# Performance work log

Measured on AMD Instinct MI355X. Metric: run time of the kernel, lower is better.

Reference implementation:

```python
import jax, jax.numpy as jnp
import numpy as np

B, C, H, W = 8, 64, 32, 32
NEG = 256
TEMP = 2.0
FACTOR = 0.8
EPS = 1e-8


def setup_inputs() -> dict:
    key = jax.random.key(0)
    k1, k2, k3, k4 = jax.random.split(key, 4)
    views_1 = jax.random.normal(k1, (B, C, H, W), dtype=jnp.float32)
    views_2 = jax.random.normal(k2, (B, C, H, W), dtype=jnp.float32)
    img = jax.random.uniform(k3, (1, 3, H, W), dtype=jnp.float32)
    neg_idx = jax.random.randint(k4, (B, 2, H * W, NEG), 0, H, dtype=jnp.int32)
    return {"views_1": views_1, "views_2": views_2, "img": img, "neg_idx": neg_idx}


def _forward(views_1, views_2, img, neg_idx):
    hw = H * W
    height = jnp.arange(hw) // W
    width = jnp.arange(hw) % W
    coords = jnp.stack([height, width]).astype(jnp.float32)  # [2, hw]
    img0 = img[0]  # [3, H, W]; original uses img[0] for EVERY batch element
    euc_norm = jnp.sqrt(jnp.asarray((H - 1) ** 2 + (W - 1) ** 2, jnp.float32))
    sqrt3 = jnp.sqrt(jnp.asarray(3.0, jnp.float32))

    center = img0[:, height, width]  # [3, hw]

    def per_sample(z1, z2, nidx):
        # nidx: [2, hw, neg]
        nf = nidx.astype(jnp.float32)
        # torch.norm with no dim => scalar Frobenius norm over [2, neg] per pixel
        d = coords[:, :, None] - nf  # [2, hw, neg]
        euc = jnp.sqrt(jnp.sum(d * d, axis=(0, 2))) / euc_norm  # [hw]
        negs = img0[:, nidx[0], nidx[1]]  # [3, hw, neg]
        rd = center[:, :, None] - negs
        rgb = jnp.sqrt(jnp.sum(rd * rd, axis=(0, 2))) / sqrt3  # [hw]
        weight = euc * FACTOR + rgb * (1.0 - FACTOR)  # [hw], constant across neg

        z1v = z1.reshape(C, hw)  # [c, hw]
        pn = z2[:, nidx[0], nidx[1]]  # [c, hw, neg]
        dot = jnp.einsum('cp,cpn->pn', z1v, pn)  # [hw, neg]
        z1sq = jnp.sum(z1v * z1v, axis=0)  # [hw]
        z1n = jnp.sqrt(z1sq)
        pnn = jnp.sqrt(jnp.sum(pn * pn, axis=0))  # [hw, neg]
        cos = dot / jnp.maximum(z1n[:, None] * pnn, EPS)  # [hw, neg]
        cos0 = z1sq / jnp.maximum(z1sq, EPS)  # [hw] (self-similarity ~ 1)

        sim_neg = jnp.minimum(jnp.abs(cos * weight[:, None]), 1.0)  # [hw, neg]
        sim0 = jnp.minimum(jnp.abs(cos0), 1.0)  # [hw]
        sim = jnp.concatenate(
            [jnp.mean(sim0)[None], jnp.mean(sim_neg, axis=0) / TEMP]
        )  # [neg+1]

        # BCELoss with target = [1, 0, ..., 0]; torch clamps log terms at -100
        logp = jnp.maximum(jnp.log(sim[0]), -100.0)
        log1m = jnp.maximum(jnp.log1p(-sim[1:]), -100.0)
        bce = -(logp + jnp.sum(log1m)) / (NEG + 1)
        return bce, sim

    bce, sims = jax.vmap(per_sample)(views_1, views_2, neg_idx)
    loss = jnp.mean(bce)
    sim_all = jnp.sum(sims, axis=0)
    return (loss, sim_all[0] / B, jnp.sum(sim_all[1:]) / NEG * TEMP / B)


def reference(views_1, views_2, img, neg_idx):
    return _forward(views_1, views_2, img, neg_idx)
```

## Files before the change

### kernel.cpp

```cpp
#include <hip/hip_runtime.h>
#include <math.h>

#define BB 8
#define CC 64
#define HH 32
#define WW 32
#define HW 1024
#define NEGN 256
#define TEMP 2.0f
#define FACTOR 0.8f
#define EPSF 1e-8f
#define PT 8

__global__ __launch_bounds__(256) void contrastive_fused(
    const float* __restrict__ z1,
    const float* __restrict__ z2,
    const float* __restrict__ img,
    const int*   __restrict__ nidx,
    float* __restrict__ accSim,
    float* __restrict__ accSim0)
{
    __shared__ float As_s[CC * PT];
    __shared__ float Dt_s[PT * HW];
    __shared__ float normq_s[HW];
    __shared__ float imgs[3 * HW];
    __shared__ float simpart[PT * NEGN];
    __shared__ float z1sqs[PT];

    const int t  = threadIdx.x;
    const int b  = blockIdx.x >> 7;
    const int p0 = (blockIdx.x & 127) * PT;

    const int lane32 = t & 31;
    const int pp_b   = t >> 5;
    const int p_b    = p0 + pp_b;

    int rr[8], cc_[8];
    const size_t nbase = ((size_t)(b * 2) * HW + p_b) * NEGN;
    #pragma unroll
    for (int j = 0; j < 8; ++j) {
        rr[j]  = nidx[nbase + lane32 + 32 * j];
        cc_[j] = nidx[nbase + (size_t)HW * NEGN + lane32 + 32 * j];
    }

    for (int i = t; i < CC * PT; i += 256) {
        const int c = i >> 3, pp = i & 7;
        As_s[i] = z1[((size_t)(b * CC + c)) * HW + p0 + pp];
    }
    for (int i = t; i < 3 * HW; i += 256) imgs[i] = img[i];
    __syncthreads();

    if (t < PT) {
        float s = 0.f;
        #pragma unroll
        for (int c = 0; c < CC; ++c) { const float v = As_s[c * PT + t]; s += v * v; }
        z1sqs[t] = s;
    }

    const float4* __restrict__ z2f4 =
        reinterpret_cast<const float4*>(z2 + (size_t)b * CC * HW);
    float4 acc[PT];
    #pragma unroll
    for (int pp = 0; pp < PT; ++pp) acc[pp] = make_float4(0.f, 0.f, 0.f, 0.f);
    float4 sq = make_float4(0.f, 0.f, 0.f, 0.f);

    #pragma unroll 8
    for (int k = 0; k < CC; ++k) {
        const float4 bv = z2f4[k * (HW / 4) + t];
        sq.x = fmaf(bv.x, bv.x, sq.x);
        sq.y = fmaf(bv.y, bv.y, sq.y);
        sq.z = fmaf(bv.z, bv.z, sq.z);
        sq.w = fmaf(bv.w, bv.w, sq.w);
        const float4 a03 = reinterpret_cast<const float4*>(As_s)[k * 2];
        const float4 a47 = reinterpret_cast<const float4*>(As_s)[k * 2 + 1];
        const float av[8] = {a03.x, a03.y, a03.z, a03.w, a47.x, a47.y, a47.z, a47.w};
        #pragma unroll
        for (int pp = 0; pp < PT; ++pp) {
            acc[pp].x = fmaf(av[pp], bv.x, acc[pp].x);
            acc[pp].y = fmaf(av[pp], bv.y, acc[pp].y);
            acc[pp].z = fmaf(av[pp], bv.z, acc[pp].z);
            acc[pp].w = fmaf(av[pp], bv.w, acc[pp].w);
        }
    }
    float4* Dt4 = reinterpret_cast<float4*>(Dt_s);
    #pragma unroll
    for (int pp = 0; pp < PT; ++pp) Dt4[pp * (HW / 4) + t] = acc[pp];
    reinterpret_cast<float4*>(normq_s)[t] =
        make_float4(sqrtf(sq.x), sqrtf(sq.y), sqrtf(sq.z), sqrtf(sq.w));
    __syncthreads();

    const float z1sq = z1sqs[pp_b];
    const float z1n  = sqrtf(z1sq);
    const float cen0 = imgs[p_b], cen1 = imgs[HW + p_b], cen2 = imgs[2 * HW + p_b];
    const float hp = (float)(p_b >> 5), wp = (float)(p_b & 31);

    float se = 0.f, sr = 0.f;
    float cosv[8];
    #pragma unroll
    for (int j = 0; j < 8; ++j) {
        const int q = rr[j] * WW + cc_[j];
        const float dh = hp - (float)rr[j], dw = wp - (float)cc_[j];
        se += dh * dh + dw * dw;
        const float d0 = cen0 - imgs[q];
        const float d1 = cen1 - imgs[HW + q];
        const float d2 = cen2 - imgs[2 * HW + q];
        sr += d0 * d0 + d1 * d1 + d2 * d2;
        const float dot = Dt_s[pp_b * HW + q];
        const float pnn = normq_s[q];
        cosv[j] = dot / fmaxf(z1n * pnn, EPSF);
    }
    #pragma unroll
    for (int off = 16; off; off >>= 1) {
        se += __shfl_xor(se, off);
        sr += __shfl_xor(sr, off);
    }
    const float euc_norm = sqrtf((float)((HH - 1) * (HH - 1) + (WW - 1) * (WW - 1)));
    const float weight = sqrtf(se) / euc_norm * FACTOR +
                         sqrtf(sr) / sqrtf(3.0f) * (1.0f - FACTOR);
    #pragma unroll
    for (int j = 0; j < 8; ++j)
        simpart[pp_b * NEGN + lane32 + 32 * j] = fminf(fabsf(cosv[j] * weight), 1.0f);
    __syncthreads();

    float s = 0.f;
    #pragma unroll
    for (int pp = 0; pp < PT; ++pp) s += simpart[pp * NEGN + t];
    atomicAdd(accSim + b * NEGN + t, s);

    if (t < PT) {
        const float c0 = z1sq / fmaxf(z1sq, EPSF);
        float s0 = fminf(fabsf(c0), 1.0f);
        #pragma unroll
        for (int off = 4; off; off >>= 1) s0 += __shfl_xor(s0, off);
        if (t == 0) atomicAdd(accSim0 + b, s0);
    }
}

__global__ __launch_bounds__(256) void finalize(
    const float* __restrict__ accSim,
    const float* __restrict__ accSim0,
    float* __restrict__ out)
{
    const int t = threadIdx.x;
    float ssum = 0.f, lsum = 0.f;
    #pragma unroll
    for (int b = 0; b < BB; ++b) {
        const float s = accSim[b * NEGN + t] * (1.0f / HW) * (1.0f / TEMP);
        ssum += s;
        lsum += fmaxf(log1pf(-s), -100.0f);
    }
    __shared__ float rs[4], rl[4];
    #pragma unroll
    for (int off = 32; off; off >>= 1) {
        ssum += __shfl_down(ssum, off);
        lsum += __shfl_down(lsum, off);
    }
    if ((t & 63) == 0) { rs[t >> 6] = ssum; rl[t >> 6] = lsum; }
    __syncthreads();

    if (t == 0) {
        const float S = rs[0] + rs[1] + rs[2] + rs[3];
        const float L = rl[0] + rl[1] + rl[2] + rl[3];
        float logpsum = 0.f, sim0sum = 0.f;
        #pragma unroll
        for (int b = 0; b < BB; ++b) {
            const float s0 = accSim0[b] * (1.0f / HW);
            sim0sum += s0;
            logpsum += fmaxf(logf(s0), -100.0f);
        }
        out[0] = -(logpsum + L) / ((float)(NEGN + 1) * (float)BB);
        out[1] = sim0sum / (float)BB;
        out[2] = S / (float)NEGN * TEMP / (float)BB;
    }
}

extern "C" void kernel_launch(void* const* d_in, const int* in_sizes, int n_in,
                              void* d_out, int out_size, void* d_ws, size_t ws_size,
                              hipStream_t stream) {
    const float* v1   = (const float*)d_in[0];
    const float* v2   = (const float*)d_in[1];
    const float* img  = (const float*)d_in[2];
    const int*   nidx = (const int*)  d_in[3];

    float* accSim  = (float*)d_ws;
    float* accSim0 = accSim + BB * NEGN;

    hipMemsetAsync(accSim, 0, (BB * NEGN + BB) * sizeof(float), stream);

    contrastive_fused<<<BB * (HW / PT), 256, 0, stream>>>(
        v1, v2, img, nidx, accSim, accSim0);
    finalize<<<1, 256, 0, stream>>>(accSim, accSim0, (float*)d_out);
}
```

Before: 106.2 us.

## Replace atomics and memset with per-tile partials and multi-block finalize

Drops the memset and the global atomicAdds. Each tile now writes its partial similarity sums to a workspace, and a finalize kernel with one block per batch reduces them, with the last block producing the outputs through an atomic counter. The change also folds the reciprocal norms into the stored dot products, removing a per-lookup divide, and reuses shared memory between the z1 tile and the sim partials. The counter is reset inside the first kernel, which depends on kernel ordering, and the finalize reads more workspace data.

```diff
diff --git a/kernel.cpp b/kernel.cpp
--- a/kernel.cpp
+++ b/kernel.cpp
@@ -11,30 +11,38 @@
 #define FACTOR 0.8f
 #define EPSF 1e-8f
 #define PT 8
+#define NTILE 128
+
+#define WS_PART   0
+#define WS_S0PART (BB * NTILE * NEGN)
+#define WS_BRES   (WS_S0PART + BB * NTILE)
+#define WS_CNT    (WS_BRES + BB * 3)
 
 __global__ __launch_bounds__(256) void contrastive_fused(
     const float* __restrict__ z1,
     const float* __restrict__ z2,
     const float* __restrict__ img,
     const int*   __restrict__ nidx,
-    float* __restrict__ accSim,
-    float* __restrict__ accSim0)
+    float* __restrict__ ws)
 {
-    __shared__ float As_s[CC * PT];
-    __shared__ float Dt_s[PT * HW];
-    __shared__ float normq_s[HW];
-    __shared__ float imgs[3 * HW];
-    __shared__ float simpart[PT * NEGN];
-    __shared__ float z1sqs[PT];
+    __shared__ float smem[2048 + PT * HW + 3 * HW + PT];
+    float* const un    = smem;
+    float* const Dt_s  = smem + 2048;
+    float* const imgs  = Dt_s + PT * HW;
+    float* const z1sqs = imgs + 3 * HW;
 
     const int t  = threadIdx.x;
     const int b  = blockIdx.x >> 7;
-    const int p0 = (blockIdx.x & 127) * PT;
+    const int tile = blockIdx.x & (NTILE - 1);
+    const int p0 = tile * PT;
 
     const int lane32 = t & 31;
     const int pp_b   = t >> 5;
     const int p_b    = p0 + pp_b;
 
+    if (blockIdx.x == 0 && t == 0)
+        ((int*)ws)[WS_CNT] = 0;
+
     int rr[8], cc_[8];
     const size_t nbase = ((size_t)(b * 2) * HW + p_b) * NEGN;
     #pragma unroll
@@ -45,7 +53,7 @@
 
     for (int i = t; i < CC * PT; i += 256) {
         const int c = i >> 3, pp = i & 7;
-        As_s[i] = z1[((size_t)(b * CC + c)) * HW + p0 + pp];
+        un[i] = z1[((size_t)(b * CC + c)) * HW + p0 + pp];
     }
     for (int i = t; i < 3 * HW; i += 256) imgs[i] = img[i];
     __syncthreads();
@@ -53,7 +61,7 @@
     if (t < PT) {
         float s = 0.f;
         #pragma unroll
-        for (int c = 0; c < CC; ++c) { const float v = As_s[c * PT + t]; s += v * v; }
+        for (int c = 0; c < CC; ++c) { const float v = un[c * PT + t]; s += v * v; }
         z1sqs[t] = s;
     }
 
@@ -71,8 +79,8 @@
         sq.y = fmaf(bv.y, bv.y, sq.y);
         sq.z = fmaf(bv.z, bv.z, sq.z);
         sq.w = fmaf(bv.w, bv.w, sq.w);
-        const float4 a03 = reinterpret_cast<const float4*>(As_s)[k * 2];
-        const float4 a47 = reinterpret_cast<const float4*>(As_s)[k * 2 + 1];
+        const float4 a03 = reinterpret_cast<const float4*>(un)[k * 2];
+        const float4 a47 = reinterpret_cast<const float4*>(un)[k * 2 + 1];
         const float av[8] = {a03.x, a03.y, a03.z, a03.w, a47.x, a47.y, a47.z, a47.w};
         #pragma unroll
         for (int pp = 0; pp < PT; ++pp) {
@@ -82,15 +90,20 @@
             acc[pp].w = fmaf(av[pp], bv.w, acc[pp].w);
         }
     }
+    const float4 rp = make_float4(
+        1.0f / fmaxf(sqrtf(sq.x), 1e-20f), 1.0f / fmaxf(sqrtf(sq.y), 1e-20f),
+        1.0f / fmaxf(sqrtf(sq.z), 1e-20f), 1.0f / fmaxf(sqrtf(sq.w), 1e-20f));
     float4* Dt4 = reinterpret_cast<float4*>(Dt_s);
     #pragma unroll
-    for (int pp = 0; pp < PT; ++pp) Dt4[pp * (HW / 4) + t] = acc[pp];
-    reinterpret_cast<float4*>(normq_s)[t] =
-        make_float4(sqrtf(sq.x), sqrtf(sq.y), sqrtf(sq.z), sqrtf(sq.w));
+    for (int pp = 0; pp < PT; ++pp) {
+        float4 v = acc[pp];
+        v.x *= rp.x; v.y *= rp.y; v.z *= rp.z; v.w *= rp.w;
+        Dt4[pp * (HW / 4) + t] = v;
+    }
     __syncthreads();
 
     const float z1sq = z1sqs[pp_b];
-    const float z1n  = sqrtf(z1sq);
+    const float rz1  = 1.0f / fmaxf(sqrtf(z1sq), 1e-20f);
     const float cen0 = imgs[p_b], cen1 = imgs[HW + p_b], cen2 = imgs[2 * HW + p_b];
     const float hp = (float)(p_b >> 5), wp = (float)(p_b & 31);
 
@@ -105,9 +118,7 @@
         const float d1 = cen1 - imgs[HW + q];
         const float d2 = cen2 - imgs[2 * HW + q];
         sr += d0 * d0 + d1 * d1 + d2 * d2;
-        const float dot = Dt_s[pp_b * HW + q];
-        const float pnn = normq_s[q];
-        cosv[j] = dot / fmaxf(z1n * pnn, EPSF);
+        cosv[j] = Dt_s[pp_b * HW + q] * rz1;
     }
     #pragma unroll
     for (int off = 16; off; off >>= 1) {
@@ -117,60 +128,79 @@
     const float euc_norm = sqrtf((float)((HH - 1) * (HH - 1) + (WW - 1) * (WW - 1)));
     const float weight = sqrtf(se) / euc_norm * FACTOR +
                          sqrtf(sr) / sqrtf(3.0f) * (1.0f - FACTOR);
+    __syncthreads();
     #pragma unroll
     for (int j = 0; j < 8; ++j)
-        simpart[pp_b * NEGN + lane32 + 32 * j] = fminf(fabsf(cosv[j] * weight), 1.0f);
+        un[pp_b * NEGN + lane32 + 32 * j] = fminf(fabsf(cosv[j] * weight), 1.0f);
     __syncthreads();
 
     float s = 0.f;
     #pragma unroll
-    for (int pp = 0; pp < PT; ++pp) s += simpart[pp * NEGN + t];
-    atomicAdd(accSim + b * NEGN + t, s);
+    for (int pp = 0; pp < PT; ++pp) s += un[pp * NEGN + t];
+    ws[WS_PART + ((size_t)(b * NTILE + tile)) * NEGN + t] = s;
 
     if (t < PT) {
         const float c0 = z1sq / fmaxf(z1sq, EPSF);
         float s0 = fminf(fabsf(c0), 1.0f);
         #pragma unroll
         for (int off = 4; off; off >>= 1) s0 += __shfl_xor(s0, off);
-        if (t == 0) atomicAdd(accSim0 + b, s0);
+        if (t == 0) ws[WS_S0PART + b * NTILE + tile] = s0;
     }
 }
 
 __global__ __launch_bounds__(256) void finalize(
-    const float* __restrict__ accSim,
-    const float* __restrict__ accSim0,
-    float* __restrict__ out)
+    float* __restrict__ ws, float* __restrict__ out)
 {
     const int t = threadIdx.x;
-    float ssum = 0.f, lsum = 0.f;
-    #pragma unroll
-    for (int b = 0; b < BB; ++b) {
-        const float s = accSim[b * NEGN + t] * (1.0f / HW) * (1.0f / TEMP);
-        ssum += s;
-        lsum += fmaxf(log1pf(-s), -100.0f);
-    }
-    __shared__ float rs[4], rl[4];
+    const int b = blockIdx.x;
+    const float* part = ws + WS_PART + (size_t)b * NTILE * NEGN;
+
+    float s_bn = 0.f;
+    #pragma unroll 8
+    for (int tile = 0; tile < NTILE; ++tile)
+        s_bn += part[(size_t)tile * NEGN + t];
+
+    const float s = s_bn * (1.0f / HW) * (1.0f / TEMP);
+    float ssum = s;
+    float lsum = fmaxf(log1pf(-s), -100.0f);
+
+    __shared__ float rs[4], rl[4], r0[2];
     #pragma unroll
     for (int off = 32; off; off >>= 1) {
         ssum += __shfl_down(ssum, off);
         lsum += __shfl_down(lsum, off);
     }
     if ((t & 63) == 0) { rs[t >> 6] = ssum; rl[t >> 6] = lsum; }
+
+    if (t < 128) {
+        float v = ws[WS_S0PART + b * NTILE + t];
+        #pragma unroll
+        for (int off = 32; off; off >>= 1) v += __shfl_down(v, off);
+        if ((t & 63) == 0) r0[t >> 6] = v;
+    }
     __syncthreads();
 
     if (t == 0) {
-        const float S = rs[0] + rs[1] + rs[2] + rs[3];
-        const float L = rl[0] + rl[1] + rl[2] + rl[3];
-        float logpsum = 0.f, sim0sum = 0.f;
-        #pragma unroll
-        for (int b = 0; b < BB; ++b) {
-            const float s0 = accSim0[b] * (1.0f / HW);
-            sim0sum += s0;
-            logpsum += fmaxf(logf(s0), -100.0f);
+        ws[WS_BRES + b * 3 + 0] = rs[0] + rs[1] + rs[2] + rs[3];
+        ws[WS_BRES + b * 3 + 1] = rl[0] + rl[1] + rl[2] + rl[3];
+        ws[WS_BRES + b * 3 + 2] = r0[0] + r0[1];
+        __threadfence();
+        const int done = atomicAdd((int*)ws + WS_CNT, 1);
+        if (done == BB - 1) {
+            __threadfence();
+            float S = 0.f, L = 0.f, logp = 0.f, s0m = 0.f;
+            #pragma unroll
+            for (int bb = 0; bb < BB; ++bb) {
+                S += ws[WS_BRES + bb * 3 + 0];
+                L += ws[WS_BRES + bb * 3 + 1];
+                const float s0 = ws[WS_BRES + bb * 3 + 2] * (1.0f / HW);
+                s0m  += s0;
+                logp += fmaxf(logf(s0), -100.0f);
+            }
+            out[0] = -(logp + L) / ((float)(NEGN + 1) * (float)BB);
+            out[1] = s0m / (float)BB;
+            out[2] = S / (float)NEGN * TEMP / (float)BB;
         }
-        out[0] = -(logpsum + L) / ((float)(NEGN + 1) * (float)BB);
-        out[1] = sim0sum / (float)BB;
-        out[2] = S / (float)NEGN * TEMP / (float)BB;
     }
 }
 
@@ -181,13 +211,8 @@
     const float* v2   = (const float*)d_in[1];
     const float* img  = (const float*)d_in[2];
     const int*   nidx = (const int*)  d_in[3];
-
-    float* accSim  = (float*)d_ws;
-    float* accSim0 = accSim + BB * NEGN;
-
-    hipMemsetAsync(accSim, 0, (BB * NEGN + BB) * sizeof(float), stream);
-
-    contrastive_fused<<<BB * (HW / PT), 256, 0, stream>>>(
-        v1, v2, img, nidx, accSim, accSim0);
-    finalize<<<1, 256, 0, stream>>>(accSim, accSim0, (float*)d_out);
+    float* ws = (float*)d_ws;
+
+    contrastive_fused<<<BB * NTILE, 256, 0, stream>>>(v1, v2, img, nidx, ws);
+    finalize<<<BB, 256, 0, stream>>>(ws, (float*)d_out);
 }
```

New measurement: 125.1 us. 1.18x slower.

## Drop image and norm staging in LDS, prescale dots by reciprocal norms, use LDS atomics

Applied to the files above, without the earlier changes.

The image is no longer copied into shared memory; it is read directly from global memory through the cache. The per-column norm array and the division are replaced by multiplying the dot products with reciprocal norms before storing them. The per-pixel partial sims are reduced with shared-memory atomics instead of a staging buffer and an extra pass. A small init kernel also replaces the memset. Together these cut LDS footprint, which may raise occupancy, and remove copy and divide work. The cost is cached global gathers and atomic contention, and the max-with-EPS clamp semantics change slightly.

```diff
diff --git a/kernel.cpp b/kernel.cpp
--- a/kernel.cpp
+++ b/kernel.cpp
@@ -11,6 +11,13 @@
 #define FACTOR 0.8f
 #define EPSF 1e-8f
 #define PT 8
+#define NTILE 128
+
+
+__global__ __launch_bounds__(256) void init_acc(float* __restrict__ acc) {
+    const int i = blockIdx.x * 256 + threadIdx.x;
+    if (i < BB * NEGN + BB) acc[i] = 0.f;
+}
 
 __global__ __launch_bounds__(256) void contrastive_fused(
     const float* __restrict__ z1,
@@ -22,14 +29,13 @@
 {
     __shared__ float As_s[CC * PT];
     __shared__ float Dt_s[PT * HW];
-    __shared__ float normq_s[HW];
-    __shared__ float imgs[3 * HW];
-    __shared__ float simpart[PT * NEGN];
+    __shared__ float nacc[NEGN];
     __shared__ float z1sqs[PT];
 
-    const int t  = threadIdx.x;
-    const int b  = blockIdx.x >> 7;
-    const int p0 = (blockIdx.x & 127) * PT;
+    const int t    = threadIdx.x;
+    const int b    = blockIdx.x >> 7;
+    const int tile = blockIdx.x & (NTILE - 1);
+    const int p0   = tile * PT;
 
     const int lane32 = t & 31;
     const int pp_b   = t >> 5;
@@ -43,11 +49,12 @@
         cc_[j] = nidx[nbase + (size_t)HW * NEGN + lane32 + 32 * j];
     }
 
+    #pragma unroll
     for (int i = t; i < CC * PT; i += 256) {
         const int c = i >> 3, pp = i & 7;
         As_s[i] = z1[((size_t)(b * CC + c)) * HW + p0 + pp];
     }
-    for (int i = t; i < 3 * HW; i += 256) imgs[i] = img[i];
+    nacc[t] = 0.f;
     __syncthreads();
 
     if (t < PT) {
@@ -82,16 +89,21 @@
             acc[pp].w = fmaf(av[pp], bv.w, acc[pp].w);
         }
     }
+    const float4 rp = make_float4(
+        1.0f / fmaxf(sqrtf(sq.x), 1e-20f), 1.0f / fmaxf(sqrtf(sq.y), 1e-20f),
+        1.0f / fmaxf(sqrtf(sq.z), 1e-20f), 1.0f / fmaxf(sqrtf(sq.w), 1e-20f));
     float4* Dt4 = reinterpret_cast<float4*>(Dt_s);
     #pragma unroll
-    for (int pp = 0; pp < PT; ++pp) Dt4[pp * (HW / 4) + t] = acc[pp];
-    reinterpret_cast<float4*>(normq_s)[t] =
-        make_float4(sqrtf(sq.x), sqrtf(sq.y), sqrtf(sq.z), sqrtf(sq.w));
+    for (int pp = 0; pp < PT; ++pp) {
+        float4 v = acc[pp];
+        v.x *= rp.x; v.y *= rp.y; v.z *= rp.z; v.w *= rp.w;
+        Dt4[pp * (HW / 4) + t] = v;
+    }
     __syncthreads();
 
     const float z1sq = z1sqs[pp_b];
-    const float z1n  = sqrtf(z1sq);
-    const float cen0 = imgs[p_b], cen1 = imgs[HW + p_b], cen2 = imgs[2 * HW + p_b];
+    const float rz1  = 1.0f / fmaxf(sqrtf(z1sq), 1e-20f);
+    const float cen0 = img[p_b], cen1 = img[HW + p_b], cen2 = img[2 * HW + p_b];
     const float hp = (float)(p_b >> 5), wp = (float)(p_b & 31);
 
     float se = 0.f, sr = 0.f;
@@ -101,13 +113,11 @@
         const int q = rr[j] * WW + cc_[j];
         const float dh = hp - (float)rr[j], dw = wp - (float)cc_[j];
         se += dh * dh + dw * dw;
-        const float d0 = cen0 - imgs[q];
-        const float d1 = cen1 - imgs[HW + q];
-        const float d2 = cen2 - imgs[2 * HW + q];
+        const float d0 = cen0 - img[q];
+        const float d1 = cen1 - img[HW + q];
+        const float d2 = cen2 - img[2 * HW + q];
         sr += d0 * d0 + d1 * d1 + d2 * d2;
-        const float dot = Dt_s[pp_b * HW + q];
-        const float pnn = normq_s[q];
-        cosv[j] = dot / fmaxf(z1n * pnn, EPSF);
+        cosv[j] = Dt_s[pp_b * HW + q] * rz1;
     }
     #pragma unroll
     for (int off = 16; off; off >>= 1) {
@@ -117,15 +127,13 @@
     const float euc_norm = sqrtf((float)((HH - 1) * (HH - 1) + (WW - 1) * (WW - 1)));
     const float weight = sqrtf(se) / euc_norm * FACTOR +
                          sqrtf(sr) / sqrtf(3.0f) * (1.0f - FACTOR);
+
     #pragma unroll
     for (int j = 0; j < 8; ++j)
-        simpart[pp_b * NEGN + lane32 + 32 * j] = fminf(fabsf(cosv[j] * weight), 1.0f);
-    __syncthreads();
-
-    float s = 0.f;
-    #pragma unroll
-    for (int pp = 0; pp < PT; ++pp) s += simpart[pp * NEGN + t];
-    atomicAdd(accSim + b * NEGN + t, s);
+        atomicAdd(&nacc[lane32 + 32 * j], fminf(fabsf(cosv[j] * weight), 1.0f));
+    __syncthreads();
+
+    atomicAdd(accSim + b * NEGN + t, nacc[t]);
 
     if (t < PT) {
         const float c0 = z1sq / fmaxf(z1sq, EPSF);
@@ -185,9 +193,8 @@
     float* accSim  = (float*)d_ws;
     float* accSim0 = accSim + BB * NEGN;
 
-    hipMemsetAsync(accSim, 0, (BB * NEGN + BB) * sizeof(float), stream);
-
-    contrastive_fused<<<BB * (HW / PT), 256, 0, stream>>>(
+    init_acc<<<(BB * NEGN + BB + 255) / 256, 256, 0, stream>>>(accSim);
+    contrastive_fused<<<BB * NTILE, 256, 0, stream>>>(
         v1, v2, img, nidx, accSim, accSim0);
     finalize<<<1, 256, 0, stream>>>(accSim, accSim0, (float*)d_out);
 }
```

New measurement: 114.8 us. +8.1%, slower.
